# Performance work log

Measured on AMD Instinct MI355X. Metric: run time of the kernel, lower is better.

## Reference

```python
import jax, jax.numpy as jnp
import numpy as np

N = 10000      # n_nodes
FEAT = 512     # n_features
HID = 256
EMB = 128
NC = 10        # n_clusters
NE = 160000    # given edge count
K = 10         # topk for topology graph


def gcn_conv(x, W, b, src, dst, n):
    """PyG GCNConv: add self-loops, symmetric D^-1/2 (A+I) D^-1/2 X W + b."""
    h = x @ W  # [n, out]
    loop = jnp.arange(n)
    s = jnp.concatenate([src, loop])
    d = jnp.concatenate([dst, loop])
    deg = jax.ops.segment_sum(jnp.ones(s.shape[0], x.dtype), d, num_segments=n)
    dinv = jnp.where(deg > 0, deg ** -0.5, 0.0)
    norm = dinv[s] * dinv[d]  # [E+n]
    out = jax.ops.segment_sum(h[s] * norm[:, None], d, num_segments=n)
    return out + b


def setup_inputs() -> dict:
    key = jax.random.key(0)
    ks = jax.random.split(key, 8)
    return {
        "x": jax.random.normal(ks[0], (N, FEAT), jnp.float32),
        "edge_index": jax.random.randint(ks[1], (2, NE), 0, N),
        "W_s1": jax.random.normal(ks[2], (FEAT, HID), jnp.float32) * 0.05,
        "b_s1": jnp.zeros((HID,), jnp.float32),
        "W_s2": jax.random.normal(ks[3], (HID, EMB), jnp.float32) * 0.05,
        "b_s2": jnp.zeros((EMB,), jnp.float32),
        "W_t1": jax.random.normal(ks[4], (FEAT, HID), jnp.float32) * 0.05,
        "b_t1": jnp.zeros((HID,), jnp.float32),
        "W_t2": jax.random.normal(ks[5], (HID, EMB), jnp.float32) * 0.05,
        "b_t2": jnp.zeros((EMB,), jnp.float32),
        "fusion_weight": jnp.float32(0.5),
        "centroids": jax.random.normal(ks[6], (NC, EMB), jnp.float32),
    }


def reference(x, edge_index, W_s1, b_s1, W_s2, b_s2, W_t1, b_t1, W_t2, b_t2,
              fusion_weight, centroids):
    src, dst = edge_index[0], edge_index[1]
    # structural branch
    z_s = gcn_conv(x, W_s1, b_s1, src, dst, N)
    z_s = gcn_conv(jax.nn.relu(z_s), W_s2, b_s2, src, dst, N)
    # topology graph: cosine-sim kNN (vectorized replacement of python loop)
    x_norm = x / jnp.maximum(jnp.linalg.norm(x, axis=1, keepdims=True), 1e-12)
    sim = x_norm @ x_norm.T                       # [N, N]
    _, topk_idx = jax.lax.top_k(sim, K)           # [N, K]
    src_t = jnp.repeat(jnp.arange(N), K - 1)
    dst_t = topk_idx[:, 1:].reshape(-1)           # skip top-1 (self)
    # topology branch
    z_t = gcn_conv(x, W_t1, b_t1, src_t, dst_t, N)
    z_t = gcn_conv(jax.nn.relu(z_t), W_t2, b_t2, src_t, dst_t, N)
    # fusion
    beta = jax.nn.sigmoid(fusion_weight)
    z = beta * z_s + (1.0 - beta) * z_t           # [N, EMB]
    # soft cluster assignment (Student-t with dist^2)
    sq = jnp.sum((z[:, None, :] - centroids[None, :, :]) ** 2, axis=-1)  # [N, NC]
    q = 1.0 / (1.0 + sq)
    q = q / jnp.sum(q, axis=1, keepdims=True)
    return (z, q)
```

## Files before the change

kernel.cpp:

```cpp
#include <hip/hip_runtime.h>
#include <math.h>

#define N_NODES 10000
#define FEAT 512
#define HID 256
#define EMB 128
#define NC 10
#define NE_EDGES 160000
#define KTOP 10
#define NNB 9

#define CAP 128
#define NSEL 24
#define TAU 0.11f
#define SAFE_VAL 0.12f
#define NTB 79
#define NPAIR 3160
#define QCAP 2048

typedef __attribute__((ext_vector_type(8))) short short8;
typedef __attribute__((ext_vector_type(4))) float f32x4;

typedef const __attribute__((address_space(1))) unsigned int* gas1_t;
typedef __attribute__((address_space(3))) unsigned int* las3_t;

__device__ __forceinline__ void gload_lds16(const void* g, void* l) {
  __builtin_amdgcn_global_load_lds((gas1_t)g, (las3_t)l, 16, 0, 0);
}

__device__ __forceinline__ unsigned short f2h(float f) {
  _Float16 h = (_Float16)f;
  return *(unsigned short*)&h;
}
__device__ __forceinline__ float h2f(unsigned short u) {
  _Float16 h = *(_Float16*)&u;
  return (float)h;
}

__device__ __forceinline__ unsigned char f2e8(float f) {
  const unsigned u = __float_as_uint(f);
  const unsigned sg = (u >> 24) & 0x80u;
  const int e = (int)((u >> 23) & 0xffu) - 127;
  const unsigned m = u & 0x7fffffu;
  if (e >= -6) {
    if (e > 8) return sg | 0x7eu;
    unsigned mant = m >> 20;
    const unsigned rest = m & 0xfffffu;
    if (rest > 0x80000u || (rest == 0x80000u && (mant & 1u))) ++mant;
    unsigned ex = (unsigned)(e + 7);
    if (mant == 8u) { mant = 0u; ++ex; }
    if (ex > 15u || (ex == 15u && mant == 7u)) return sg | 0x7eu;
    return sg | (ex << 3) | mant;
  }
  const float af = fabsf(f);
  const int q = (int)(af * 512.0f + 0.5f);
  if (q > 7) return sg | 0x08u;
  return sg | (unsigned)q;
}

__global__ void k_norms(const float* __restrict__ x, unsigned char* __restrict__ xn8,
                        unsigned short* __restrict__ xf, double* __restrict__ rinv) {
  const int row = blockIdx.x;
  const int t = threadIdx.x;
  const float4 v = *(const float4*)(x + (size_t)row * FEAT + t * 4);
  double s = (double)v.x * v.x + (double)v.y * v.y + (double)v.z * v.z + (double)v.w * v.w;
  __shared__ double red[128];
  red[t] = s;
  __syncthreads();
  for (int o = 64; o > 0; o >>= 1) {
    if (t < o) red[t] += red[t + o];
    __syncthreads();
  }
  const double inv = 1.0 / fmax(sqrt(red[0]), 1e-12);
  const float finv = (float)inv;
  unsigned short hf[4] = {f2h(v.x), f2h(v.y), f2h(v.z), f2h(v.w)};
  *(uint2*)(xf + (size_t)row * FEAT + t * 4) = *(uint2*)hf;
  unsigned char e8[4] = {f2e8(v.x * finv), f2e8(v.y * finv), f2e8(v.z * finv),
                         f2e8(v.w * finv)};
  *(unsigned int*)(xn8 + (size_t)row * FEAT + t * 4) = *(unsigned int*)e8;
  if (t == 0) rinv[row] = inv;
}

__global__ void k_wt(const float* __restrict__ W, unsigned short* __restrict__ Wt, int K, int N) {
  const int idx = blockIdx.x * 256 + threadIdx.x;
  if (idx < K * N) {
    const int n = idx / K, k = idx % K;
    Wt[idx] = f2h(W[(size_t)k * N + n]);
  }
}

__global__ __launch_bounds__(256) void k_simgemm(const unsigned char* __restrict__ xn8,
                                                 unsigned int* __restrict__ cap_buf,
                                                 int* __restrict__ cnt_row) {
  __shared__ __align__(16) unsigned char As[3][8192];
  __shared__ __align__(16) unsigned char Bs[3][8192];
  __shared__ int hn;

  const int t = threadIdx.x;
  const int lane = t & 63;
  const int w = t >> 6;
  const int lr = lane & 15;
  const int lk = lane >> 4;
  const int wr = (w >> 1) * 64, wc = (w & 1) * 64;

  const int bid = (blockIdx.x & 7) * 395 + (blockIdx.x >> 3);
  int bi = (int)((159.0 - sqrt(25281.0 - 8.0 * (double)bid)) * 0.5);
  while ((bi + 1) * NTB - (bi + 1) * bi / 2 <= bid) ++bi;
  while (bi * NTB - bi * (bi - 1) / 2 > bid) --bi;
  const int bj = bi + (bid - (bi * NTB - bi * (bi - 1) / 2));
  const int arow0 = bi * 128;
  const int bcol0 = bj * 128;

  auto stage = [&](int s, int k0) {
#pragma unroll
    for (int it = 0; it < 2; ++it) {
      const int slot = it * 256 + t;
      const int r = slot >> 2;
      const int qs = (slot & 3) ^ ((r >> 1) & 3);
      {
        const int gr = min(arow0 + r, N_NODES - 1);
        gload_lds16(xn8 + (size_t)gr * FEAT + k0 + qs * 16, &As[s][(it * 256 + w * 64) * 16]);
      }
      {
        const int gc = min(bcol0 + r, N_NODES - 1);
        gload_lds16(xn8 + (size_t)gc * FEAT + k0 + qs * 16, &Bs[s][(it * 256 + w * 64) * 16]);
      }
    }
  };

  f32x4 acc[4][4];
#pragma unroll
  for (int m = 0; m < 4; ++m)
#pragma unroll
    for (int n = 0; n < 4; ++n) acc[m][n] = (f32x4){0.f, 0.f, 0.f, 0.f};

  stage(0, 0);
  stage(1, 64);

  const int NT = FEAT / 64;
  int cur = 0, nxt = 2;
  for (int kt = 0; kt < NT; ++kt) {
    if (kt + 2 < NT) {
      stage(nxt, (kt + 2) * 64);
      asm volatile("s_waitcnt vmcnt(8)" ::: "memory");
    } else if (kt + 1 < NT) {
      asm volatile("s_waitcnt vmcnt(4)" ::: "memory");
    } else {
      asm volatile("s_waitcnt vmcnt(0)" ::: "memory");
    }
    __builtin_amdgcn_sched_barrier(0);
    __builtin_amdgcn_s_barrier();
    const unsigned char* Ab = As[cur];
    const unsigned char* Bb = Bs[cur];
    long av[2][4], bv[2][4];
#pragma unroll
    for (int h = 0; h < 2; ++h) {
#pragma unroll
      for (int m = 0; m < 4; ++m) {
        const int row = wr + m * 16 + lr;
        const int sl = (h * 2 + (lk >> 1)) ^ ((row >> 1) & 3);
        av[h][m] = *(const long*)(Ab + row * 64 + sl * 16 + (lk & 1) * 8);
      }
#pragma unroll
      for (int n = 0; n < 4; ++n) {
        const int row = wc + n * 16 + lr;
        const int sl = (h * 2 + (lk >> 1)) ^ ((row >> 1) & 3);
        bv[h][n] = *(const long*)(Bb + row * 64 + sl * 16 + (lk & 1) * 8);
      }
    }
    __builtin_amdgcn_s_setprio(1);
#pragma unroll
    for (int h = 0; h < 2; ++h)
#pragma unroll
      for (int m = 0; m < 4; ++m)
#pragma unroll
        for (int n = 0; n < 4; ++n)
          acc[m][n] =
              __builtin_amdgcn_mfma_f32_16x16x32_fp8_fp8(av[h][m], bv[h][n], acc[m][n], 0, 0, 0);
    __builtin_amdgcn_s_setprio(0);
    asm volatile("" ::: "memory");
    if (kt + 1 < NT) __builtin_amdgcn_s_barrier();
    cur = (cur == 2) ? 0 : cur + 1;
    nxt = (nxt == 2) ? 0 : nxt + 1;
  }

  __syncthreads();
  unsigned* hq = (unsigned*)&As[0][0];
  if (t == 0) hn = 0;
  __syncthreads();
  const bool offdiag = (bi != bj);
#pragma unroll
  for (int m = 0; m < 4; ++m) {
    const int lrow0 = wr + m * 16 + lk * 4;
#pragma unroll
    for (int n = 0; n < 4; ++n) {
      const int lcol = wc + n * 16 + lr;
#pragma unroll
      for (int q = 0; q < 4; ++q) {
        const float v = acc[m][n][q];
        if (v > TAU && (arow0 + lrow0 + q) < N_NODES && (bcol0 + lcol) < N_NODES) {
          const int p = atomicAdd(&hn, 1);
          if (p < QCAP)
            hq[p] = ((unsigned)f2h(v) << 16) | ((unsigned)(lrow0 + q) << 7) | (unsigned)lcol;
        }
      }
    }
  }
  __syncthreads();
  const int H = hn;
  if (H <= QCAP) {
    for (int e = t; e < H; e += 256) {
      const unsigned pk = hq[e];
      const int gr = arow0 + (int)((pk >> 7) & 127u);
      const int gc = bcol0 + (int)(pk & 127u);
      const unsigned hv = pk >> 16;
      {
        const int pos = atomicAdd(&cnt_row[gr], 1);
        if (pos < CAP) cap_buf[(size_t)gr * CAP + pos] = (hv << 16) | (unsigned)gc;
      }
      if (offdiag) {
        const int pos = atomicAdd(&cnt_row[gc], 1);
        if (pos < CAP) cap_buf[(size_t)gc * CAP + pos] = (hv << 16) | (unsigned)gr;
      }
    }
  } else {
#pragma unroll
    for (int m = 0; m < 4; ++m) {
      const int rb = arow0 + wr + m * 16 + lk * 4;
#pragma unroll
      for (int n = 0; n < 4; ++n) {
        const int gc = bcol0 + wc + n * 16 + lr;
        if (gc < N_NODES) {
#pragma unroll
          for (int q = 0; q < 4; ++q) {
            const float v = acc[m][n][q];
            const int gr = rb + q;
            if (v > TAU && gr < N_NODES) {
              const unsigned short hv = f2h(v);
              {
                const int pos = atomicAdd(&cnt_row[gr], 1);
                if (pos < CAP)
                  cap_buf[(size_t)gr * CAP + pos] = ((unsigned)hv << 16) | (unsigned)gc;
              }
              if (offdiag) {
                const int pos = atomicAdd(&cnt_row[gc], 1);
                if (pos < CAP)
                  cap_buf[(size_t)gc * CAP + pos] = ((unsigned)hv << 16) | (unsigned)gr;
              }
            }
          }
        }
      }
    }
  }
}

__global__ __launch_bounds__(256) void k_knn(const float* __restrict__ x,
                                             const double* __restrict__ rinv,
                                             const unsigned int* __restrict__ cap_buf,
                                             const int* __restrict__ cnt_row,
                                             int* __restrict__ nb, int* __restrict__ flags) {
  const int i = blockIdx.x;
  const int t = threadIdx.x;
  const int lane = t & 63;
  const int wave = t >> 6;
  __shared__ unsigned pp[CAP];
  __shared__ int sel[NSEL];
  __shared__ float xi[FEAT];
  __shared__ double dsv[NSEL];
  __shared__ int safe_cnt;

  const int cnt = cnt_row[i];
  if (cnt > CAP || cnt < NSEL) {
    if (t == 0) flags[i] = 1;
    return;
  }
  if (t == 0) { flags[i] = 0; safe_cnt = 0; }
  const int L = cnt;
  if (t < L) pp[t] = cap_buf[(size_t)i * CAP + t];
  xi[t] = x[(size_t)i * FEAT + t];
  xi[t + 256] = x[(size_t)i * FEAT + t + 256];
  __syncthreads();

  if (t < L) {
    const unsigned p = pp[t];
    if (h2f((unsigned short)(p >> 16)) >= SAFE_VAL) atomicAdd(&safe_cnt, 1);
    int rk = 0;
    for (int j = 0; j < L; ++j) rk += (pp[j] > p);
    if (rk < NSEL) sel[rk] = (int)(p & 0xffffu);
  }
  __syncthreads();
  if (safe_cnt < KTOP) {
    if (t == 0) flags[i] = 1;
    return;
  }

  const double ri = rinv[i];
  const float4 v0 = *(const float4*)(xi + lane * 8);
  const float4 v1 = *(const float4*)(xi + lane * 8 + 4);
#pragma unroll
  for (int q = 0; q < 6; ++q) {
    const int c = wave * 6 + q;
    const int ci = sel[c];
    const float4* xr = (const float4*)(x + (size_t)ci * FEAT);
    const float4 u0 = xr[lane * 2];
    const float4 u1 = xr[lane * 2 + 1];
    double s = (double)u0.x * (double)v0.x + (double)u0.y * (double)v0.y +
               (double)u0.z * (double)v0.z + (double)u0.w * (double)v0.w +
               (double)u1.x * (double)v1.x + (double)u1.y * (double)v1.y +
               (double)u1.z * (double)v1.z + (double)u1.w * (double)v1.w;
#pragma unroll
    for (int off = 1; off < 64; off <<= 1) s += __shfl_xor(s, off);
    if (lane == 0) dsv[c] = s * ri * rinv[ci];
  }
  __syncthreads();

  if (t < NSEL) {
    const double v = dsv[t];
    const int id = sel[t];
    int rk = 0;
    for (int j = 0; j < NSEL; ++j)
      rk += (dsv[j] > v) || (dsv[j] == v && sel[j] < id);
    if (rk >= 1 && rk < KTOP) nb[(size_t)i * NNB + (rk - 1)] = id;
  }
}

__global__ __launch_bounds__(256) void k_fallback(const float* __restrict__ x,
                                                  const double* __restrict__ rinv,
                                                  const int* __restrict__ flags,
                                                  int* __restrict__ nb) {
  const int i = blockIdx.x;
  if (!flags[i]) return;
  const int t = threadIdx.x;
  __shared__ float xi[FEAT];
  __shared__ double cval[256];
  __shared__ double bestv[NNB];
  __shared__ int besti[NNB];
  for (int k = t; k < FEAT; k += 256) xi[k] = x[(size_t)i * FEAT + k];
  if (t < NNB) { bestv[t] = -1e300; besti[t] = 0x7fffffff; }
  __syncthreads();
  const double ri = rinv[i];
  for (int c0 = 0; c0 < N_NODES; c0 += 256) {
    const int c = c0 + t;
    double s = -1e300;
    if (c < N_NODES && c != i) {
      s = 0.0;
      for (int k = 0; k < FEAT; ++k) s += (double)xi[k] * (double)x[(size_t)c * FEAT + k];
      s *= ri * rinv[c];
    }
    cval[t] = s;
    __syncthreads();
    if (t == 0) {
      for (int j = 0; j < 256; ++j) {
        const int c2 = c0 + j;
        const double v = cval[j];
        if (v == -1e300) continue;
        int pos = NNB;
        for (int q = 0; q < NNB; ++q) {
          if (v > bestv[q] || (v == bestv[q] && c2 < besti[q])) { pos = q; break; }
        }
        if (pos < NNB) {
          for (int q = NNB - 1; q > pos; --q) { bestv[q] = bestv[q - 1]; besti[q] = besti[q - 1]; }
          bestv[pos] = v; besti[pos] = c2;
        }
      }
    }
    __syncthreads();
  }
  if (t < NNB) nb[(size_t)i * NNB + t] = besti[t];
}

__global__ void k_zero3(int* __restrict__ a, int* __restrict__ b, int* __restrict__ c) {
  const int i = blockIdx.x * blockDim.x + threadIdx.x;
  if (i < N_NODES) { a[i] = 0; b[i] = 0; c[i] = 0; }
}

__global__ void k_count(const int* __restrict__ dsts, int ne, int* __restrict__ cnt) {
  const int e = blockIdx.x * blockDim.x + threadIdx.x;
  if (e < ne) atomicAdd(&cnt[dsts[e]], 1);
}

__global__ void k_scan2(const int* __restrict__ cnt0, int* __restrict__ off0,
                        int* __restrict__ cur0, float* __restrict__ dinv0,
                        const int* __restrict__ cnt1, int* __restrict__ off1,
                        int* __restrict__ cur1, float* __restrict__ dinv1) {
  const int* cnt = blockIdx.x ? cnt1 : cnt0;
  int* off = blockIdx.x ? off1 : off0;
  int* cur = blockIdx.x ? cur1 : cur0;
  float* dinv = blockIdx.x ? dinv1 : dinv0;
  __shared__ int buf[1024];
  __shared__ int base_s;
  const int t = threadIdx.x;
  if (t == 0) base_s = 0;
  __syncthreads();
  for (int b0 = 0; b0 < N_NODES; b0 += 1024) {
    const int i = b0 + t;
    const int v = (i < N_NODES) ? cnt[i] : 0;
    buf[t] = v;
    __syncthreads();
    for (int o = 1; o < 1024; o <<= 1) {
      const int add = (t >= o) ? buf[t - o] : 0;
      __syncthreads();
      buf[t] += add;
      __syncthreads();
    }
    const int incl = buf[t];
    const int base = base_s;
    if (i < N_NODES) {
      const int excl = base + incl - v;
      off[i] = excl;
      cur[i] = excl;
      dinv[i] = rsqrtf((float)(v + 1));
    }
    __syncthreads();
    if (t == 1023) base_s = base + buf[1023];
    __syncthreads();
  }
  if (t == 0) off[N_NODES] = base_s;
}

__global__ void k_scatter_s(const int* __restrict__ src, const int* __restrict__ dst, int ne,
                            int* __restrict__ cur, int* __restrict__ csr) {
  const int e = blockIdx.x * blockDim.x + threadIdx.x;
  if (e < ne) {
    const int p = atomicAdd(&cur[dst[e]], 1);
    csr[p] = src[e];
  }
}

__global__ void k_scatter_t(const int* __restrict__ nb, int* __restrict__ cur,
                            int* __restrict__ csr) {
  const int e = blockIdx.x * blockDim.x + threadIdx.x;
  if (e < N_NODES * NNB) {
    const int i = e / NNB;
    const int v = nb[e];
    const int p = atomicAdd(&cur[v], 1);
    csr[p] = i;
  }
}

__global__ __launch_bounds__(256) void k_fgemm2(const unsigned short* __restrict__ A0,
                                                const unsigned short* __restrict__ A1,
                                                const unsigned short* __restrict__ Bt0,
                                                const unsigned short* __restrict__ Bt1,
                                                unsigned short* __restrict__ C0,
                                                unsigned short* __restrict__ C1,
                                                int M, int K, int N) {
  __shared__ __align__(16) unsigned short As[3][4096];
  __shared__ __align__(16) unsigned short Bs[3][4096];
  const int t = threadIdx.x;
  const int lane = t & 63, w = t >> 6;
  const int lr = lane & 15, lk = lane >> 4;
  const int wr = (w >> 1) * 64, wc = (w & 1) * 64;
  const int nbn = N >> 7;
  const int half = blockIdx.y / nbn;
  const unsigned short* A = half ? A1 : A0;
  const unsigned short* Bt = half ? Bt1 : Bt0;
  unsigned short* C = half ? C1 : C0;
  const int arow0 = blockIdx.x * 128, bcol0 = (blockIdx.y % nbn) * 128;

  auto stage = [&](int s, int k0) {
#pragma unroll
    for (int it = 0; it < 2; ++it) {
      const int slot = it * 256 + w * 64 + lane;
      const int r = slot >> 2;
      const int qs = (slot & 3) ^ ((r >> 1) & 3);
      {
        const int gr = min(arow0 + r, M - 1);
        gload_lds16(A + (size_t)gr * K + k0 + qs * 8, &As[s][(it * 256 + w * 64) * 8]);
      }
      {
        const int gc = min(bcol0 + r, N - 1);
        gload_lds16(Bt + (size_t)gc * K + k0 + qs * 8, &Bs[s][(it * 256 + w * 64) * 8]);
      }
    }
  };

  f32x4 acc[4][4];
#pragma unroll
  for (int m = 0; m < 4; ++m)
#pragma unroll
    for (int n = 0; n < 4; ++n) acc[m][n] = (f32x4){0.f, 0.f, 0.f, 0.f};

  stage(0, 0);
  if (K > 32) stage(1, 32);

  const int NT = K >> 5;
  int cur = 0, nxt = 2;
  for (int kt = 0; kt < NT; ++kt) {
    if (kt + 2 < NT) {
      stage(nxt, (kt + 2) << 5);
      asm volatile("s_waitcnt vmcnt(8)" ::: "memory");
    } else if (kt + 1 < NT) {
      asm volatile("s_waitcnt vmcnt(4)" ::: "memory");
    } else {
      asm volatile("s_waitcnt vmcnt(0)" ::: "memory");
    }
    __builtin_amdgcn_sched_barrier(0);
    __builtin_amdgcn_s_barrier();
    const unsigned short* Ab = As[cur];
    const unsigned short* Bb = Bs[cur];
    short8 a[4], b[4];
#pragma unroll
    for (int m = 0; m < 4; ++m) {
      const int row = wr + m * 16 + lr;
      a[m] = *(const short8*)(Ab + (((row << 2) | (lk ^ ((row >> 1) & 3))) << 3));
    }
#pragma unroll
    for (int n = 0; n < 4; ++n) {
      const int row = wc + n * 16 + lr;
      b[n] = *(const short8*)(Bb + (((row << 2) | (lk ^ ((row >> 1) & 3))) << 3));
    }
    __builtin_amdgcn_s_setprio(1);
#pragma unroll
    for (int m = 0; m < 4; ++m)
#pragma unroll
      for (int n = 0; n < 4; ++n)
        acc[m][n] = __builtin_amdgcn_mfma_f32_16x16x32_f16(a[m], b[n], acc[m][n], 0, 0, 0);
    __builtin_amdgcn_s_setprio(0);
    asm volatile("" ::: "memory");
    if (kt + 1 < NT) __builtin_amdgcn_s_barrier();
    cur = (cur == 2) ? 0 : cur + 1;
    nxt = (nxt == 2) ? 0 : nxt + 1;
  }

#pragma unroll
  for (int m = 0; m < 4; ++m) {
    const int rb = arow0 + wr + m * 16 + lk * 4;
#pragma unroll
    for (int n = 0; n < 4; ++n) {
      const int gc = bcol0 + wc + n * 16 + lr;
#pragma unroll
      for (int q = 0; q < 4; ++q) {
        const int gm = rb + q;
        if (gm < M) C[(size_t)gm * N + gc] = f2h(acc[m][n][q]);
      }
    }
  }
}

__global__ void k_agg_h(const unsigned short* __restrict__ h, const float* __restrict__ bias,
                        const float* __restrict__ dinv, const int* __restrict__ off,
                        const int* __restrict__ csr, unsigned short* __restrict__ out) {
  const int v = blockIdx.x;
  const int c = threadIdx.x;
  const float dv = dinv[v];
  float acc = h2f(h[(size_t)v * HID + c]) * dv;
  const int s0 = off[v], s1 = off[v + 1];
  int e = s0;
  for (; e + 1 < s1; e += 2) {
    const int sa = csr[e], sb = csr[e + 1];
    const float ha = h2f(h[(size_t)sa * HID + c]), hb = h2f(h[(size_t)sb * HID + c]);
    acc += ha * dinv[sa] + hb * dinv[sb];
  }
  if (e < s1) {
    const int sa = csr[e];
    acc += h2f(h[(size_t)sa * HID + c]) * dinv[sa];
  }
  acc = acc * dv + bias[c];
  out[(size_t)v * HID + c] = f2h(fmaxf(acc, 0.f));
}

__global__ void k_agg(const unsigned short* __restrict__ h, const float* __restrict__ bias,
                      const float* __restrict__ dinv, const int* __restrict__ off,
                      const int* __restrict__ csr, float* __restrict__ out) {
  const int v = blockIdx.x;
  const int c = threadIdx.x;
  const float dv = dinv[v];
  float acc = h2f(h[(size_t)v * EMB + c]) * dv;
  const int s0 = off[v], s1 = off[v + 1];
  int e = s0;
  for (; e + 1 < s1; e += 2) {
    const int sa = csr[e], sb = csr[e + 1];
    const float ha = h2f(h[(size_t)sa * EMB + c]), hb = h2f(h[(size_t)sb * EMB + c]);
    acc += ha * dinv[sa] + hb * dinv[sb];
  }
  if (e < s1) {
    const int sa = csr[e];
    acc += h2f(h[(size_t)sa * EMB + c]) * dinv[sa];
  }
  out[(size_t)v * EMB + c] = acc * dv + bias[c];
}

__global__ void k_fuse(const float* __restrict__ zs, const float* __restrict__ zt,
                       const float* __restrict__ fw, const float* __restrict__ cent,
                       float* __restrict__ out_z, float* __restrict__ out_q) {
  const int v = blockIdx.x;
  const int t = threadIdx.x;
  __shared__ float zsh[EMB];
  __shared__ float cs[NC][EMB];
  __shared__ float qv[NC];
  __shared__ float qs;
  for (int k = t; k < NC * EMB; k += 128) ((float*)cs)[k] = cent[k];
  const float beta = 1.f / (1.f + expf(-fw[0]));
  const float z = beta * zs[(size_t)v * EMB + t] + (1.f - beta) * zt[(size_t)v * EMB + t];
  out_z[(size_t)v * EMB + t] = z;
  zsh[t] = z;
  __syncthreads();
  if (t < NC) {
    float s = 0.f;
    for (int c = 0; c < EMB; ++c) {
      const float d = zsh[c] - cs[t][c];
      s += d * d;
    }
    qv[t] = 1.f / (1.f + s);
  }
  __syncthreads();
  if (t == 0) {
    float s = 0.f;
    for (int k = 0; k < NC; ++k) s += qv[k];
    qs = s;
  }
  __syncthreads();
  if (t < NC) out_q[(size_t)v * NC + t] = qv[t] / qs;
}

extern "C" void kernel_launch(void* const* d_in, const int* in_sizes, int n_in, void* d_out,
                              int out_size, void* d_ws, size_t ws_size, hipStream_t stream) {
  const float* x = (const float*)d_in[0];
  const int* ei = (const int*)d_in[1];
  const float* W_s1 = (const float*)d_in[2];
  const float* b_s1 = (const float*)d_in[3];
  const float* W_s2 = (const float*)d_in[4];
  const float* b_s2 = (const float*)d_in[5];
  const float* W_t1 = (const float*)d_in[6];
  const float* b_t1 = (const float*)d_in[7];
  const float* W_t2 = (const float*)d_in[8];
  const float* b_t2 = (const float*)d_in[9];
  const float* fw = (const float*)d_in[10];
  const float* cent = (const float*)d_in[11];
  float* out_z = (float*)d_out;
  float* out_q = out_z + (size_t)N_NODES * EMB;

  char* w = (char*)d_ws;
  size_t o = 0;
  auto alloc = [&](size_t bytes) -> void* {
    void* p = w + o;
    o += (bytes + 255) & ~(size_t)255;
    return p;
  };
  unsigned char* xn8 = (unsigned char*)alloc((size_t)N_NODES * FEAT * 2);
  unsigned short* h1_s = (unsigned short*)xn8;
  unsigned short* xf = (unsigned short*)alloc((size_t)N_NODES * FEAT * 2);
  unsigned short* h2_s = xf;
  unsigned short* h2_t = xf + (size_t)N_NODES * EMB;
  double* rinv = (double*)alloc((size_t)N_NODES * 8);
  unsigned int* cap_buf = (unsigned int*)alloc((size_t)N_NODES * CAP * 4);
  unsigned short* r1_s = (unsigned short*)cap_buf;
  unsigned short* r1_t = (unsigned short*)alloc((size_t)N_NODES * HID * 2);
  unsigned short* h1_t = (unsigned short*)alloc((size_t)N_NODES * HID * 2);
  float* z_s = (float*)alloc((size_t)N_NODES * EMB * 4);
  float* z_t = (float*)alloc((size_t)N_NODES * EMB * 4);
  int* nb = (int*)alloc((size_t)N_NODES * NNB * 4);
  int* cnt_s = (int*)alloc((size_t)N_NODES * 4);
  int* off_s = (int*)alloc((size_t)(N_NODES + 1) * 4);
  int* cur_s = (int*)alloc((size_t)N_NODES * 4);
  float* dinv_s = (float*)alloc((size_t)N_NODES * 4);
  int* cnt_t = (int*)alloc((size_t)N_NODES * 4);
  int* off_t = (int*)alloc((size_t)(N_NODES + 1) * 4);
  int* cur_t = (int*)alloc((size_t)N_NODES * 4);
  float* dinv_t = (float*)alloc((size_t)N_NODES * 4);
  int* csr_s = (int*)alloc((size_t)NE_EDGES * 4);
  int* csr_t = (int*)alloc((size_t)N_NODES * NNB * 4);
  int* cnt_row = (int*)alloc((size_t)N_NODES * 4);
  int* flags = (int*)alloc((size_t)N_NODES * 4);
  unsigned short* Wt_s1 = (unsigned short*)alloc((size_t)FEAT * HID * 2);
  unsigned short* Wt_t1 = (unsigned short*)alloc((size_t)FEAT * HID * 2);
  unsigned short* Wt_s2 = (unsigned short*)alloc((size_t)HID * EMB * 2);
  unsigned short* Wt_t2 = (unsigned short*)alloc((size_t)HID * EMB * 2);

  const int* e_src = ei;
  const int* e_dst = ei + NE_EDGES;

  k_norms<<<N_NODES, 128, 0, stream>>>(x, xn8, xf, rinv);
  k_wt<<<(FEAT * HID + 255) / 256, 256, 0, stream>>>(W_s1, Wt_s1, FEAT, HID);
  k_wt<<<(FEAT * HID + 255) / 256, 256, 0, stream>>>(W_t1, Wt_t1, FEAT, HID);
  k_wt<<<(HID * EMB + 255) / 256, 256, 0, stream>>>(W_s2, Wt_s2, HID, EMB);
  k_wt<<<(HID * EMB + 255) / 256, 256, 0, stream>>>(W_t2, Wt_t2, HID, EMB);
  k_zero3<<<(N_NODES + 255) / 256, 256, 0, stream>>>(cnt_s, cnt_t, cnt_row);
  k_count<<<(NE_EDGES + 255) / 256, 256, 0, stream>>>(e_dst, NE_EDGES, cnt_s);
  k_simgemm<<<NPAIR, 256, 0, stream>>>(xn8, cap_buf, cnt_row);
  k_knn<<<N_NODES, 256, 0, stream>>>(x, rinv, cap_buf, cnt_row, nb, flags);
  k_fallback<<<N_NODES, 256, 0, stream>>>(x, rinv, flags, nb);
  k_count<<<(N_NODES * NNB + 255) / 256, 256, 0, stream>>>(nb, N_NODES * NNB, cnt_t);
  k_scan2<<<2, 1024, 0, stream>>>(cnt_s, off_s, cur_s, dinv_s, cnt_t, off_t, cur_t, dinv_t);
  k_scatter_s<<<(NE_EDGES + 255) / 256, 256, 0, stream>>>(e_src, e_dst, NE_EDGES, cur_s, csr_s);
  k_scatter_t<<<(N_NODES * NNB + 255) / 256, 256, 0, stream>>>(nb, cur_t, csr_t);
  {
    dim3 g1(NTB, 2 * (HID / 128));
    k_fgemm2<<<g1, 256, 0, stream>>>(xf, xf, Wt_s1, Wt_t1, h1_s, h1_t, N_NODES, FEAT, HID);
  }
  k_agg_h<<<N_NODES, HID, 0, stream>>>(h1_s, b_s1, dinv_s, off_s, csr_s, r1_s);
  k_agg_h<<<N_NODES, HID, 0, stream>>>(h1_t, b_t1, dinv_t, off_t, csr_t, r1_t);
  {
    dim3 g2(NTB, 2 * (EMB / 128));
    k_fgemm2<<<g2, 256, 0, stream>>>(r1_s, r1_t, Wt_s2, Wt_t2, h2_s, h2_t, N_NODES, HID, EMB);
  }
  k_agg<<<N_NODES, EMB, 0, stream>>>(h2_s, b_s2, dinv_s, off_s, csr_s, z_s);
  k_agg<<<N_NODES, EMB, 0, stream>>>(h2_t, b_t2, dinv_t, off_t, csr_t, z_t);
  k_fuse<<<N_NODES, 128, 0, stream>>>(z_s, z_t, fw, cent, out_z, out_q);
}
```

Baseline: 357.3 us.

## Fuse small kernels, block xn8 by K-chunks, and use a wave-shuffle scan

Stores the fp8 normalized features in a K-blocked layout ([k/64][node][64]) so each sim-GEMM stage load reads a contiguous 64-byte row slice. It merges the four weight-transpose launches into one, folds the topology-degree count into the kNN and fallback kernels via atomics, and merges both first-layer aggregations into a single 2D grid. The second-layer aggregations are fused with the fusion/soft-assignment kernel, which removes the z_s/z_t intermediates. The scan now uses wave shuffles instead of a barrier-heavy LDS Hillis-Steele loop. Together these cut launch count, global round trips and barriers, at the cost of more atomics in k_knn.

```diff
diff --git a/kernel.cpp b/kernel.cpp
--- a/kernel.cpp
+++ b/kernel.cpp
@@ -77,15 +77,40 @@
   *(uint2*)(xf + (size_t)row * FEAT + t * 4) = *(uint2*)hf;
   unsigned char e8[4] = {f2e8(v.x * finv), f2e8(v.y * finv), f2e8(v.z * finv),
                          f2e8(v.w * finv)};
-  *(unsigned int*)(xn8 + (size_t)row * FEAT + t * 4) = *(unsigned int*)e8;
+  const int kb = t >> 4;
+  const int ko = (t * 4) & 63;
+  *(unsigned int*)(xn8 + ((size_t)kb * N_NODES + row) * 64 + ko) = *(unsigned int*)e8;
   if (t == 0) rinv[row] = inv;
 }
 
-__global__ void k_wt(const float* __restrict__ W, unsigned short* __restrict__ Wt, int K, int N) {
-  const int idx = blockIdx.x * 256 + threadIdx.x;
-  if (idx < K * N) {
-    const int n = idx / K, k = idx % K;
-    Wt[idx] = f2h(W[(size_t)k * N + n]);
+__global__ void k_wtall(const float* __restrict__ W_s1, const float* __restrict__ W_t1,
+                        const float* __restrict__ W_s2, const float* __restrict__ W_t2,
+                        unsigned short* __restrict__ Wt_s1, unsigned short* __restrict__ Wt_t1,
+                        unsigned short* __restrict__ Wt_s2, unsigned short* __restrict__ Wt_t2) {
+  int idx = blockIdx.x * 256 + threadIdx.x;
+  const int n1 = FEAT * HID;
+  const int n2 = HID * EMB;
+  if (idx < n1) {
+    const int n = idx / FEAT, k = idx % FEAT;
+    Wt_s1[idx] = f2h(W_s1[(size_t)k * HID + n]);
+    return;
+  }
+  idx -= n1;
+  if (idx < n1) {
+    const int n = idx / FEAT, k = idx % FEAT;
+    Wt_t1[idx] = f2h(W_t1[(size_t)k * HID + n]);
+    return;
+  }
+  idx -= n1;
+  if (idx < n2) {
+    const int n = idx / HID, k = idx % HID;
+    Wt_s2[idx] = f2h(W_s2[(size_t)k * EMB + n]);
+    return;
+  }
+  idx -= n2;
+  if (idx < n2) {
+    const int n = idx / HID, k = idx % HID;
+    Wt_t2[idx] = f2h(W_t2[(size_t)k * EMB + n]);
   }
 }
 
@@ -112,6 +137,7 @@
   const int bcol0 = bj * 128;
 
   auto stage = [&](int s, int k0) {
+    const unsigned char* kbp = xn8 + (size_t)(k0 >> 6) * N_NODES * 64;
 #pragma unroll
     for (int it = 0; it < 2; ++it) {
       const int slot = it * 256 + t;
@@ -119,11 +145,11 @@
       const int qs = (slot & 3) ^ ((r >> 1) & 3);
       {
         const int gr = min(arow0 + r, N_NODES - 1);
-        gload_lds16(xn8 + (size_t)gr * FEAT + k0 + qs * 16, &As[s][(it * 256 + w * 64) * 16]);
+        gload_lds16(kbp + (size_t)gr * 64 + qs * 16, &As[s][(it * 256 + w * 64) * 16]);
       }
       {
         const int gc = min(bcol0 + r, N_NODES - 1);
-        gload_lds16(xn8 + (size_t)gc * FEAT + k0 + qs * 16, &Bs[s][(it * 256 + w * 64) * 16]);
+        gload_lds16(kbp + (size_t)gc * 64 + qs * 16, &Bs[s][(it * 256 + w * 64) * 16]);
       }
     }
   };
@@ -259,7 +285,8 @@
                                              const double* __restrict__ rinv,
                                              const unsigned int* __restrict__ cap_buf,
                                              const int* __restrict__ cnt_row,
-                                             int* __restrict__ nb, int* __restrict__ flags) {
+                                             int* __restrict__ nb, int* __restrict__ flags,
+                                             int* __restrict__ cnt_t) {
   const int i = blockIdx.x;
   const int t = threadIdx.x;
   const int lane = t & 63;
@@ -321,14 +348,18 @@
     int rk = 0;
     for (int j = 0; j < NSEL; ++j)
       rk += (dsv[j] > v) || (dsv[j] == v && sel[j] < id);
-    if (rk >= 1 && rk < KTOP) nb[(size_t)i * NNB + (rk - 1)] = id;
+    if (rk >= 1 && rk < KTOP) {
+      nb[(size_t)i * NNB + (rk - 1)] = id;
+      atomicAdd(&cnt_t[id], 1);
+    }
   }
 }
 
 __global__ __launch_bounds__(256) void k_fallback(const float* __restrict__ x,
                                                   const double* __restrict__ rinv,
                                                   const int* __restrict__ flags,
-                                                  int* __restrict__ nb) {
+                                                  int* __restrict__ nb,
+                                                  int* __restrict__ cnt_t) {
   const int i = blockIdx.x;
   if (!flags[i]) return;
   const int t = threadIdx.x;
@@ -367,7 +398,10 @@
     }
     __syncthreads();
   }
-  if (t < NNB) nb[(size_t)i * NNB + t] = besti[t];
+  if (t < NNB) {
+    nb[(size_t)i * NNB + t] = besti[t];
+    atomicAdd(&cnt_t[besti[t]], 1);
+  }
 }
 
 __global__ void k_zero3(int* __restrict__ a, int* __restrict__ b, int* __restrict__ c) {
@@ -388,32 +422,44 @@
   int* off = blockIdx.x ? off1 : off0;
   int* cur = blockIdx.x ? cur1 : cur0;
   float* dinv = blockIdx.x ? dinv1 : dinv0;
-  __shared__ int buf[1024];
-  __shared__ int base_s;
+  __shared__ int wsum[16];
+  __shared__ int woff[16];
+  __shared__ int base_s, tot_s;
   const int t = threadIdx.x;
+  const int lane = t & 63, wid = t >> 6;
   if (t == 0) base_s = 0;
   __syncthreads();
   for (int b0 = 0; b0 < N_NODES; b0 += 1024) {
     const int i = b0 + t;
     const int v = (i < N_NODES) ? cnt[i] : 0;
-    buf[t] = v;
+    int inc = v;
+#pragma unroll
+    for (int o = 1; o < 64; o <<= 1) {
+      const int u = __shfl_up(inc, o, 64);
+      if (lane >= o) inc += u;
+    }
+    if (lane == 63) wsum[wid] = inc;
     __syncthreads();
-    for (int o = 1; o < 1024; o <<= 1) {
-      const int add = (t >= o) ? buf[t - o] : 0;
-      __syncthreads();
-      buf[t] += add;
-      __syncthreads();
-    }
-    const int incl = buf[t];
-    const int base = base_s;
+    if (wid == 0) {
+      const int ws = (lane < 16) ? wsum[lane] : 0;
+      int wi = ws;
+#pragma unroll
+      for (int o = 1; o < 16; o <<= 1) {
+        const int u = __shfl_up(wi, o, 64);
+        if (lane >= o) wi += u;
+      }
+      if (lane < 16) woff[lane] = wi - ws;
+      if (lane == 15) tot_s = wi;
+    }
+    __syncthreads();
     if (i < N_NODES) {
-      const int excl = base + incl - v;
+      const int excl = base_s + woff[wid] + (inc - v);
       off[i] = excl;
       cur[i] = excl;
       dinv[i] = rsqrtf((float)(v + 1));
     }
     __syncthreads();
-    if (t == 1023) base_s = base + buf[1023];
+    if (t == 0) base_s += tot_s;
     __syncthreads();
   }
   if (t == 0) off[N_NODES] = base_s;
@@ -539,9 +585,20 @@
   }
 }
 
-__global__ void k_agg_h(const unsigned short* __restrict__ h, const float* __restrict__ bias,
-                        const float* __restrict__ dinv, const int* __restrict__ off,
-                        const int* __restrict__ csr, unsigned short* __restrict__ out) {
+__global__ void k_agg_h2(const unsigned short* __restrict__ h0,
+                         const unsigned short* __restrict__ h1,
+                         const float* __restrict__ bias0, const float* __restrict__ bias1,
+                         const float* __restrict__ dinv0, const float* __restrict__ dinv1,
+                         const int* __restrict__ off0, const int* __restrict__ off1,
+                         const int* __restrict__ csr0, const int* __restrict__ csr1,
+                         unsigned short* __restrict__ out0, unsigned short* __restrict__ out1) {
+  const int br = blockIdx.y;
+  const unsigned short* h = br ? h1 : h0;
+  const float* bias = br ? bias1 : bias0;
+  const float* dinv = br ? dinv1 : dinv0;
+  const int* off = br ? off1 : off0;
+  const int* csr = br ? csr1 : csr0;
+  unsigned short* out = br ? out1 : out0;
   const int v = blockIdx.x;
   const int c = threadIdx.x;
   const float dv = dinv[v];
@@ -561,58 +618,75 @@
   out[(size_t)v * HID + c] = f2h(fmaxf(acc, 0.f));
 }
 
-__global__ void k_agg(const unsigned short* __restrict__ h, const float* __restrict__ bias,
-                      const float* __restrict__ dinv, const int* __restrict__ off,
-                      const int* __restrict__ csr, float* __restrict__ out) {
+__global__ void k_aggfuse(const unsigned short* __restrict__ h2_s,
+                          const unsigned short* __restrict__ h2_t,
+                          const float* __restrict__ b_s2, const float* __restrict__ b_t2,
+                          const float* __restrict__ dinv_s, const int* __restrict__ off_s,
+                          const int* __restrict__ csr_s, const float* __restrict__ dinv_t,
+                          const int* __restrict__ off_t, const int* __restrict__ csr_t,
+                          const float* __restrict__ fw, const float* __restrict__ cent,
+                          float* __restrict__ out_z, float* __restrict__ out_q) {
   const int v = blockIdx.x;
   const int c = threadIdx.x;
-  const float dv = dinv[v];
-  float acc = h2f(h[(size_t)v * EMB + c]) * dv;
-  const int s0 = off[v], s1 = off[v + 1];
-  int e = s0;
-  for (; e + 1 < s1; e += 2) {
-    const int sa = csr[e], sb = csr[e + 1];
-    const float ha = h2f(h[(size_t)sa * EMB + c]), hb = h2f(h[(size_t)sb * EMB + c]);
-    acc += ha * dinv[sa] + hb * dinv[sb];
-  }
-  if (e < s1) {
-    const int sa = csr[e];
-    acc += h2f(h[(size_t)sa * EMB + c]) * dinv[sa];
-  }
-  out[(size_t)v * EMB + c] = acc * dv + bias[c];
-}
-
-__global__ void k_fuse(const float* __restrict__ zs, const float* __restrict__ zt,
-                       const float* __restrict__ fw, const float* __restrict__ cent,
-                       float* __restrict__ out_z, float* __restrict__ out_q) {
-  const int v = blockIdx.x;
-  const int t = threadIdx.x;
   __shared__ float zsh[EMB];
   __shared__ float cs[NC][EMB];
   __shared__ float qv[NC];
   __shared__ float qs;
-  for (int k = t; k < NC * EMB; k += 128) ((float*)cs)[k] = cent[k];
+  for (int k = c; k < NC * EMB; k += 128) ((float*)cs)[k] = cent[k];
+  float zs, zt;
+  {
+    const float dv = dinv_s[v];
+    float acc = h2f(h2_s[(size_t)v * EMB + c]) * dv;
+    const int s0 = off_s[v], s1 = off_s[v + 1];
+    int e = s0;
+    for (; e + 1 < s1; e += 2) {
+      const int sa = csr_s[e], sb = csr_s[e + 1];
+      acc += h2f(h2_s[(size_t)sa * EMB + c]) * dinv_s[sa] +
+             h2f(h2_s[(size_t)sb * EMB + c]) * dinv_s[sb];
+    }
+    if (e < s1) {
+      const int sa = csr_s[e];
+      acc += h2f(h2_s[(size_t)sa * EMB + c]) * dinv_s[sa];
+    }
+    zs = acc * dv + b_s2[c];
+  }
+  {
+    const float dv = dinv_t[v];
+    float acc = h2f(h2_t[(size_t)v * EMB + c]) * dv;
+    const int s0 = off_t[v], s1 = off_t[v + 1];
+    int e = s0;
+    for (; e + 1 < s1; e += 2) {
+      const int sa = csr_t[e], sb = csr_t[e + 1];
+      acc += h2f(h2_t[(size_t)sa * EMB + c]) * dinv_t[sa] +
+             h2f(h2_t[(size_t)sb * EMB + c]) * dinv_t[sb];
+    }
+    if (e < s1) {
+      const int sa = csr_t[e];
+      acc += h2f(h2_t[(size_t)sa * EMB + c]) * dinv_t[sa];
+    }
+    zt = acc * dv + b_t2[c];
+  }
   const float beta = 1.f / (1.f + expf(-fw[0]));
-  const float z = beta * zs[(size_t)v * EMB + t] + (1.f - beta) * zt[(size_t)v * EMB + t];
-  out_z[(size_t)v * EMB + t] = z;
-  zsh[t] = z;
-  __syncthreads();
-  if (t < NC) {
+  const float z = beta * zs + (1.f - beta) * zt;
+  out_z[(size_t)v * EMB + c] = z;
+  zsh[c] = z;
+  __syncthreads();
+  if (c < NC) {
     float s = 0.f;
-    for (int c = 0; c < EMB; ++c) {
-      const float d = zsh[c] - cs[t][c];
+    for (int k = 0; k < EMB; ++k) {
+      const float d = zsh[k] - cs[c][k];
       s += d * d;
     }
-    qv[t] = 1.f / (1.f + s);
-  }
-  __syncthreads();
-  if (t == 0) {
+    qv[c] = 1.f / (1.f + s);
+  }
+  __syncthreads();
+  if (c == 0) {
     float s = 0.f;
     for (int k = 0; k < NC; ++k) s += qv[k];
     qs = s;
   }
   __syncthreads();
-  if (t < NC) out_q[(size_t)v * NC + t] = qv[t] / qs;
+  if (c < NC) out_q[(size_t)v * NC + c] = qv[c] / qs;
 }
 
 extern "C" void kernel_launch(void* const* d_in, const int* in_sizes, int n_in, void* d_out,
@@ -649,8 +723,6 @@
   unsigned short* r1_s = (unsigned short*)cap_buf;
   unsigned short* r1_t = (unsigned short*)alloc((size_t)N_NODES * HID * 2);
   unsigned short* h1_t = (unsigned short*)alloc((size_t)N_NODES * HID * 2);
-  float* z_s = (float*)alloc((size_t)N_NODES * EMB * 4);
-  float* z_t = (float*)alloc((size_t)N_NODES * EMB * 4);
   int* nb = (int*)alloc((size_t)N_NODES * NNB * 4);
   int* cnt_s = (int*)alloc((size_t)N_NODES * 4);
   int* off_s = (int*)alloc((size_t)(N_NODES + 1) * 4);
@@ -673,16 +745,16 @@
   const int* e_dst = ei + NE_EDGES;
 
   k_norms<<<N_NODES, 128, 0, stream>>>(x, xn8, xf, rinv);
-  k_wt<<<(FEAT * HID + 255) / 256, 256, 0, stream>>>(W_s1, Wt_s1, FEAT, HID);
-  k_wt<<<(FEAT * HID + 255) / 256, 256, 0, stream>>>(W_t1, Wt_t1, FEAT, HID);
-  k_wt<<<(HID * EMB + 255) / 256, 256, 0, stream>>>(W_s2, Wt_s2, HID, EMB);
-  k_wt<<<(HID * EMB + 255) / 256, 256, 0, stream>>>(W_t2, Wt_t2, HID, EMB);
+  {
+    const int tot = 2 * FEAT * HID + 2 * HID * EMB;
+    k_wtall<<<(tot + 255) / 256, 256, 0, stream>>>(W_s1, W_t1, W_s2, W_t2, Wt_s1, Wt_t1, Wt_s2,
+                                                   Wt_t2);
+  }
   k_zero3<<<(N_NODES + 255) / 256, 256, 0, stream>>>(cnt_s, cnt_t, cnt_row);
   k_count<<<(NE_EDGES + 255) / 256, 256, 0, stream>>>(e_dst, NE_EDGES, cnt_s);
   k_simgemm<<<NPAIR, 256, 0, stream>>>(xn8, cap_buf, cnt_row);
-  k_knn<<<N_NODES, 256, 0, stream>>>(x, rinv, cap_buf, cnt_row, nb, flags);
-  k_fallback<<<N_NODES, 256, 0, stream>>>(x, rinv, flags, nb);
-  k_count<<<(N_NODES * NNB + 255) / 256, 256, 0, stream>>>(nb, N_NODES * NNB, cnt_t);
+  k_knn<<<N_NODES, 256, 0, stream>>>(x, rinv, cap_buf, cnt_row, nb, flags, cnt_t);
+  k_fallback<<<N_NODES, 256, 0, stream>>>(x, rinv, flags, nb, cnt_t);
   k_scan2<<<2, 1024, 0, stream>>>(cnt_s, off_s, cur_s, dinv_s, cnt_t, off_t, cur_t, dinv_t);
   k_scatter_s<<<(NE_EDGES + 255) / 256, 256, 0, stream>>>(e_src, e_dst, NE_EDGES, cur_s, csr_s);
   k_scatter_t<<<(N_NODES * NNB + 255) / 256, 256, 0, stream>>>(nb, cur_t, csr_t);
@@ -690,13 +762,15 @@
     dim3 g1(NTB, 2 * (HID / 128));
     k_fgemm2<<<g1, 256, 0, stream>>>(xf, xf, Wt_s1, Wt_t1, h1_s, h1_t, N_NODES, FEAT, HID);
   }
-  k_agg_h<<<N_NODES, HID, 0, stream>>>(h1_s, b_s1, dinv_s, off_s, csr_s, r1_s);
-  k_agg_h<<<N_NODES, HID, 0, stream>>>(h1_t, b_t1, dinv_t, off_t, csr_t, r1_t);
+  {
+    dim3 ga(N_NODES, 2);
+    k_agg_h2<<<ga, HID, 0, stream>>>(h1_s, h1_t, b_s1, b_t1, dinv_s, dinv_t, off_s, off_t, csr_s,
+                                     csr_t, r1_s, r1_t);
+  }
   {
     dim3 g2(NTB, 2 * (EMB / 128));
     k_fgemm2<<<g2, 256, 0, stream>>>(r1_s, r1_t, Wt_s2, Wt_t2, h2_s, h2_t, N_NODES, HID, EMB);
   }
-  k_agg<<<N_NODES, EMB, 0, stream>>>(h2_s, b_s2, dinv_s, off_s, csr_s, z_s);
-  k_agg<<<N_NODES, EMB, 0, stream>>>(h2_t, b_t2, dinv_t, off_t, csr_t, z_t);
-  k_fuse<<<N_NODES, 128, 0, stream>>>(z_s, z_t, fw, cent, out_z, out_q);
-}
+  k_aggfuse<<<N_NODES, EMB, 0, stream>>>(h2_s, h2_t, b_s2, b_t2, dinv_s, off_s, csr_s, dinv_t,
+                                         off_t, csr_t, fw, cent, out_z, out_q);
+}
```

Result: faster. 333.5 us (-6.7%).
